# Kernel tuning notes

Hardware: AMD Instinct MI355X
Metric: run time of the kernel (lower is better)

The kernel has to match this reference:

```python
import jax, jax.numpy as jnp
import numpy as np

N_NODES = 50000
N_EDGES = 800000
IN_CH = 128
HID = 64
HEADS = 4
OUT_CH = 12
NEG_SLOPE = 0.2


def setup_inputs() -> dict:
    key = jax.random.key(0)
    ks = jax.random.split(key, 16)
    s = 0.05
    F1 = HEADS * HID  # 256
    return {
        "x": jax.random.normal(ks[0], (N_NODES, IN_CH), jnp.float32),
        "edge_index": jax.random.randint(ks[1], (2, N_EDGES), 0, N_NODES, jnp.int64 if jax.config.jax_enable_x64 else jnp.int32),
        # GAT layer 1 params
        "W1": jax.random.normal(ks[2], (IN_CH, F1), jnp.float32) * s,
        "att_src1": jax.random.normal(ks[3], (HEADS, HID), jnp.float32) * s,
        "att_dst1": jax.random.normal(ks[4], (HEADS, HID), jnp.float32) * s,
        "b1": jnp.zeros((F1,), jnp.float32),
        # GAT layer 2 params
        "W2": jax.random.normal(ks[5], (F1, F1), jnp.float32) * s,
        "att_src2": jax.random.normal(ks[6], (HEADS, HID), jnp.float32) * s,
        "att_dst2": jax.random.normal(ks[7], (HEADS, HID), jnp.float32) * s,
        "b2": jnp.zeros((F1,), jnp.float32),
        # temporal Conv1d(F1 -> HID, k=3, pad=1)
        "conv_w": jax.random.normal(ks[8], (HID, F1, 3), jnp.float32) * s,
        "conv_b": jnp.zeros((HID,), jnp.float32),
        # final Linear(HID -> OUT_CH)
        "lin_w": jax.random.normal(ks[9], (HID, OUT_CH), jnp.float32) * s,
        "lin_b": jnp.zeros((OUT_CH,), jnp.float32),
    }


def _gat_layer(x, src, dst, W, a_src, a_dst, bias):
    # x: [N, Fin]; src/dst: [E] (self-loops already included)
    h = (x @ W).reshape(x.shape[0], HEADS, HID)          # [N, H, C]
    alpha_s = jnp.sum(h * a_src[None], axis=-1)          # [N, H]
    alpha_d = jnp.sum(h * a_dst[None], axis=-1)          # [N, H]
    e = jax.nn.leaky_relu(alpha_s[src] + alpha_d[dst], NEG_SLOPE)  # [E, H]
    # segment softmax over destination nodes
    m = jax.ops.segment_max(e, dst, num_segments=N_NODES)          # [N, H]
    ex = jnp.exp(e - m[dst])
    denom = jax.ops.segment_sum(ex, dst, num_segments=N_NODES)
    alpha = ex / (denom[dst] + 1e-16)                    # [E, H]
    msg = h[src] * alpha[:, :, None]                     # [E, H, C]
    out = jax.ops.segment_sum(msg, dst, num_segments=N_NODES)      # [N, H, C]
    return out.reshape(N_NODES, HEADS * HID) + bias


def reference(x, edge_index, W1, att_src1, att_dst1, b1, W2, att_src2, att_dst2, b2, conv_w, conv_b, lin_w, lin_b):
    # add self loops (PyG GATConv default)
    loops = jnp.arange(N_NODES, dtype=edge_index.dtype)
    src = jnp.concatenate([edge_index[0], loops])
    dst = jnp.concatenate([edge_index[1], loops])

    h = jax.nn.relu(_gat_layer(x, src, dst, W1, att_src1, att_dst1, b1))
    h = jax.nn.relu(_gat_layer(h, src, dst, W2, att_src2, att_dst2, b2))

    # temporal Conv1d over the node axis: [1, F1, N] -> [1, HID, N]
    inp = h.T[None]                                      # [1, F1, N]
    y = jax.lax.conv_general_dilated(inp, conv_w, (1,), [(1, 1)],
                                     dimension_numbers=("NCH", "OIH", "NCH"))
    y = jax.nn.relu(y + conv_b[None, :, None])           # [1, HID, N]
    out = y[0].T @ lin_w + lin_b                         # [N, OUT_CH]
    return out
```

## Files before the change

kernel.cpp:

```cpp
#include <hip/hip_runtime.h>
#include <hip/hip_bf16.h>

#define N_NODES 50000
#define N_EDGES 800000
#define E_TOT   (N_EDGES + N_NODES)
#define IN_CH   128
#define HID     64
#define HEADS   4
#define F1      256
#define OUT_CH  12
#define NEG_SLOPE 0.2f
#define CAP     256

typedef __attribute__((ext_vector_type(8))) short  bf16x8;
typedef __attribute__((ext_vector_type(4))) float  f32x4;

__device__ __forceinline__ float leaky(float x) { return x > 0.f ? x : NEG_SLOPE * x; }

__device__ __forceinline__ unsigned short tob(float f) {
    unsigned u = __float_as_uint(f);
    u += 0x7fffu + ((u >> 16) & 1u);
    return (unsigned short)(u >> 16);
}
__device__ __forceinline__ float fromb(unsigned short s) {
    return __uint_as_float(((unsigned)s) << 16);
}

__global__ void k_zero(int* p, int n) {
    int i = blockIdx.x * blockDim.x + threadIdx.x;
    if (i < n) p[i] = 0;
}

__global__ void k_count(const int* __restrict__ ei, int* __restrict__ counts) {
    int i = blockIdx.x * blockDim.x + threadIdx.x;
    if (i >= E_TOT) return;
    int dst = (i < N_EDGES) ? ei[N_EDGES + i] : (i - N_EDGES);
    atomicAdd(&counts[dst], 1);
}

__global__ __launch_bounds__(1024) void k_scan(const int* __restrict__ counts,
                                               int* __restrict__ rowptr,
                                               int* __restrict__ cursor) {
    __shared__ int wsum[16];
    __shared__ int carrysh;
    const int lane = threadIdx.x & 63, w = threadIdx.x >> 6;
    if (threadIdx.x == 0) carrysh = 0;
    __syncthreads();
    for (int base = 0; base < N_NODES; base += 1024) {
        int i = base + threadIdx.x;
        int v = (i < N_NODES) ? counts[i] : 0;
        int s = v;
        #pragma unroll
        for (int off = 1; off < 64; off <<= 1) {
            int t = __shfl_up(s, off);
            if (lane >= off) s += t;
        }
        if (lane == 63) wsum[w] = s;
        __syncthreads();
        int woff = 0;
        for (int j = 0; j < w; ++j) woff += wsum[j];
        int incl = carrysh + woff + s;
        if (i < N_NODES) { rowptr[i] = incl - v; cursor[i] = incl - v; }
        __syncthreads();
        if (threadIdx.x == 1023) carrysh = incl;
        __syncthreads();
    }
    if (threadIdx.x == 0) rowptr[N_NODES] = carrysh;
}

__global__ void k_fill(const int* __restrict__ ei, int* __restrict__ cursor,
                       int* __restrict__ csr_src) {
    int i = blockIdx.x * blockDim.x + threadIdx.x;
    if (i >= E_TOT) return;
    int src, dst;
    if (i < N_EDGES) { src = ei[i]; dst = ei[N_EDGES + i]; }
    else             { src = dst = i - N_EDGES; }
    int pos = atomicAdd(&cursor[dst], 1);
    csr_src[pos] = src;
}

__global__ void k_cast4(const float* __restrict__ in, unsigned short* __restrict__ out, int n4) {
    int i = blockIdx.x * blockDim.x + threadIdx.x;
    if (i >= n4) return;
    float4 v = *(const float4*)&in[i * 4];
    ushort4 o;
    o.x = tob(v.x); o.y = tob(v.y); o.z = tob(v.z); o.w = tob(v.w);
    *(ushort4*)&out[i * 4] = o;
}

__global__ void k_prep_wt(const float* __restrict__ W, unsigned short* __restrict__ WT,
                          int K, int N) {
    int idx = blockIdx.x * blockDim.x + threadIdx.x;
    if (idx >= K * N) return;
    int n = idx / K, k = idx % K;
    WT[idx] = tob(W[(size_t)k * N + n]);
}

__global__ void k_prep_cw(const float* __restrict__ CW, unsigned short* __restrict__ BT) {
    int idx = blockIdx.x * blockDim.x + threadIdx.x;
    if (idx >= 64 * 768) return;
    int o = idx / 768, kk = idx % 768;
    int kseg = kk >> 8, c = kk & 255;
    BT[idx] = tob(CW[((size_t)o * 256 + c) * 3 + kseg]);
}

__global__ __launch_bounds__(256) void k_gemm_bf16(const unsigned short* __restrict__ A,
                                                   const unsigned short* __restrict__ BT,
                                                   unsigned short* __restrict__ C,
                                                   int M, int K) {
    __shared__ unsigned short As[128][40];
    __shared__ unsigned short Bs[128][40];
    const int t    = threadIdx.x;
    const int lane = t & 63, wave = t >> 6;
    const int wr = wave >> 1, wc = wave & 1;
    const int row0 = blockIdx.y * 128, col0 = blockIdx.x * 128;
    const int r = t & 127, half = t >> 7;
    const int l15 = lane & 15, kg = lane >> 4;

    f32x4 acc[4][4];
    #pragma unroll
    for (int m = 0; m < 4; ++m)
        #pragma unroll
        for (int n = 0; n < 4; ++n) acc[m][n] = 0.f;

    for (int k0 = 0; k0 < K; k0 += 32) {
        int ar = row0 + r;
        uint4 av0 = make_uint4(0, 0, 0, 0), av1 = make_uint4(0, 0, 0, 0);
        if (ar < M) {
            const unsigned short* ap = &A[(size_t)ar * K + k0 + half * 16];
            av0 = *(const uint4*)ap;
            av1 = *(const uint4*)(ap + 8);
        }
        *(uint4*)&As[r][half * 16]     = av0;
        *(uint4*)&As[r][half * 16 + 8] = av1;
        const unsigned short* bp = &BT[(size_t)(col0 + r) * K + k0 + half * 16];
        uint4 bv0 = *(const uint4*)bp;
        uint4 bv1 = *(const uint4*)(bp + 8);
        *(uint4*)&Bs[r][half * 16]     = bv0;
        *(uint4*)&Bs[r][half * 16 + 8] = bv1;
        __syncthreads();
        bf16x8 af[4], bf[4];
        #pragma unroll
        for (int m = 0; m < 4; ++m) af[m] = *(const bf16x8*)&As[wr * 64 + m * 16 + l15][kg * 8];
        #pragma unroll
        for (int n = 0; n < 4; ++n) bf[n] = *(const bf16x8*)&Bs[wc * 64 + n * 16 + l15][kg * 8];
        #pragma unroll
        for (int m = 0; m < 4; ++m)
            #pragma unroll
            for (int n = 0; n < 4; ++n)
                acc[m][n] = __builtin_amdgcn_mfma_f32_16x16x32_bf16(af[m], bf[n], acc[m][n], 0, 0, 0);
        __syncthreads();
    }
    #pragma unroll
    for (int m = 0; m < 4; ++m) {
        #pragma unroll
        for (int j = 0; j < 4; ++j) {
            int row = row0 + wr * 64 + m * 16 + (lane >> 4) * 4 + j;
            if (row < M) {
                #pragma unroll
                for (int n = 0; n < 4; ++n)
                    C[(size_t)row * F1 + col0 + wc * 64 + n * 16 + l15] = tob(acc[m][n][j]);
            }
        }
    }
}

__global__ __launch_bounds__(256) void k_attn(const unsigned short* __restrict__ H,
                                              const float* __restrict__ a_src,
                                              const float* __restrict__ a_dst,
                                              float* __restrict__ oS,
                                              float* __restrict__ oD) {
    int lane = threadIdx.x & 63, wid = threadIdx.x >> 6;
    int node = blockIdx.x * 4 + wid;
    int head = lane >> 4, cc = (lane & 15) * 4;
    ushort4 hv4 = *(const ushort4*)&H[(size_t)node * F1 + lane * 4];
    float h0 = fromb(hv4.x), h1 = fromb(hv4.y), h2 = fromb(hv4.z), h3 = fromb(hv4.w);
    float4 sv = *(const float4*)&a_src[head * HID + cc];
    float4 dv = *(const float4*)&a_dst[head * HID + cc];
    float s = h0 * sv.x + h1 * sv.y + h2 * sv.z + h3 * sv.w;
    float d = h0 * dv.x + h1 * dv.y + h2 * dv.z + h3 * dv.w;
    #pragma unroll
    for (int off = 1; off < 16; off <<= 1) {
        s += __shfl_xor(s, off);
        d += __shfl_xor(d, off);
    }
    if ((lane & 15) == 0) { oS[node * 4 + head] = s; oD[node * 4 + head] = d; }
}

__global__ __launch_bounds__(256) void k_agg(const unsigned short* __restrict__ H,
                                             const float* __restrict__ aS,
                                             const float* __restrict__ aD,
                                             const int* __restrict__ rowptr,
                                             const int* __restrict__ csr,
                                             const float* __restrict__ bias,
                                             unsigned short* __restrict__ O) {
    __shared__ float wlds[4][CAP][4];
    int lane = threadIdx.x & 63, wid = threadIdx.x >> 6;
    int node = blockIdx.x * 4 + wid;
    int beg = rowptr[node], end = rowptr[node + 1];

    float4 adv = *(const float4*)&aD[node * 4];
    float ad[4] = { adv.x, adv.y, adv.z, adv.w };
    float m[4] = { -1e30f, -1e30f, -1e30f, -1e30f };
    float s[4] = { 0.f, 0.f, 0.f, 0.f };

    for (int j = beg + lane; j < end; j += 64) {
        int src = csr[j];
        float4 asv = *(const float4*)&aS[src * 4];
        float as4[4] = { asv.x, asv.y, asv.z, asv.w };
        #pragma unroll
        for (int h = 0; h < 4; ++h) {
            float e  = leaky(as4[h] + ad[h]);
            float mn = fmaxf(m[h], e);
            s[h] = s[h] * __expf(m[h] - mn) + __expf(e - mn);
            m[h] = mn;
        }
    }
    #pragma unroll
    for (int off = 1; off < 64; off <<= 1) {
        #pragma unroll
        for (int h = 0; h < 4; ++h) {
            float mo = __shfl_xor(m[h], off);
            float so = __shfl_xor(s[h], off);
            float mn = fmaxf(m[h], mo);
            s[h] = s[h] * __expf(m[h] - mn) + so * __expf(mo - mn);
            m[h] = mn;
        }
    }
    float inv4[4];
    #pragma unroll
    for (int h = 0; h < 4; ++h) inv4[h] = 1.f / (s[h] + 1e-16f);

    for (int j = beg + lane, idx = lane; j < end && idx < CAP; j += 64, idx += 64) {
        int src = csr[j];
        float4 asv = *(const float4*)&aS[src * 4];
        float4 w4;
        w4.x = __expf(leaky(asv.x + ad[0]) - m[0]) * inv4[0];
        w4.y = __expf(leaky(asv.y + ad[1]) - m[1]) * inv4[1];
        w4.z = __expf(leaky(asv.z + ad[2]) - m[2]) * inv4[2];
        w4.w = __expf(leaky(asv.w + ad[3]) - m[3]) * inv4[3];
        *(float4*)&wlds[wid][idx][0] = w4;
    }

    int   hl   = lane >> 4;
    float mh   = m[hl];
    float invh = inv4[hl];
    float adh  = ad[hl];
    float a0 = 0.f, a1 = 0.f, a2 = 0.f, a3 = 0.f;
    int deg  = end - beg;
    int degc = deg < CAP ? deg : CAP;
    for (int idx = 0; idx < degc; ++idx) {
        int src = csr[beg + idx];
        float w = wlds[wid][idx][hl];
        ushort4 hv = *(const ushort4*)&H[(size_t)src * F1 + lane * 4];
        a0 += w * fromb(hv.x); a1 += w * fromb(hv.y);
        a2 += w * fromb(hv.z); a3 += w * fromb(hv.w);
    }
    for (int idx = CAP; idx < deg; ++idx) {
        int src = csr[beg + idx];
        float e = leaky(aS[src * 4 + hl] + adh);
        float w = __expf(e - mh) * invh;
        ushort4 hv = *(const ushort4*)&H[(size_t)src * F1 + lane * 4];
        a0 += w * fromb(hv.x); a1 += w * fromb(hv.y);
        a2 += w * fromb(hv.z); a3 += w * fromb(hv.w);
    }
    float4 bv = *(const float4*)&bias[lane * 4];
    ushort4 o;
    o.x = tob(fmaxf(a0 + bv.x, 0.f));
    o.y = tob(fmaxf(a1 + bv.y, 0.f));
    o.z = tob(fmaxf(a2 + bv.z, 0.f));
    o.w = tob(fmaxf(a3 + bv.w, 0.f));
    *(ushort4*)&O[(size_t)node * F1 + lane * 4] = o;
}

__global__ __launch_bounds__(256) void k_conv(const unsigned short* __restrict__ H,
                                              const unsigned short* __restrict__ BcT,
                                              const float* __restrict__ CB,
                                              float* __restrict__ Y) {
    __shared__ unsigned short As[128][40];
    __shared__ unsigned short Bs[64][40];
    const int t    = threadIdx.x;
    const int lane = t & 63, wave = t >> 6;
    const int row0 = blockIdx.x * 128;
    const int r = t & 127, half = t >> 7;
    const int l15 = lane & 15, kg = lane >> 4;

    f32x4 acc[2][4];
    #pragma unroll
    for (int m = 0; m < 2; ++m)
        #pragma unroll
        for (int n = 0; n < 4; ++n) acc[m][n] = 0.f;

    for (int k0 = 0; k0 < 768; k0 += 32) {
        int kseg = k0 >> 8;
        int cbase = (k0 & 255) + half * 16;
        int gr = row0 + r + kseg - 1;
        uint4 av0 = make_uint4(0, 0, 0, 0), av1 = make_uint4(0, 0, 0, 0);
        if (gr >= 0 && gr < N_NODES) {
            const unsigned short* hp = &H[(size_t)gr * F1 + cbase];
            av0 = *(const uint4*)hp;
            av1 = *(const uint4*)(hp + 8);
        }
        *(uint4*)&As[r][half * 16]     = av0;
        *(uint4*)&As[r][half * 16 + 8] = av1;
        if (t < 128) {
            int br = t & 63, bh = t >> 6;
            const unsigned short* bp = &BcT[(size_t)br * 768 + k0 + bh * 16];
            uint4 bv0 = *(const uint4*)bp;
            uint4 bv1 = *(const uint4*)(bp + 8);
            *(uint4*)&Bs[br][bh * 16]     = bv0;
            *(uint4*)&Bs[br][bh * 16 + 8] = bv1;
        }
        __syncthreads();
        bf16x8 af[2], bf[4];
        #pragma unroll
        for (int m = 0; m < 2; ++m) af[m] = *(const bf16x8*)&As[wave * 32 + m * 16 + l15][kg * 8];
        #pragma unroll
        for (int n = 0; n < 4; ++n) bf[n] = *(const bf16x8*)&Bs[n * 16 + l15][kg * 8];
        #pragma unroll
        for (int m = 0; m < 2; ++m)
            #pragma unroll
            for (int n = 0; n < 4; ++n)
                acc[m][n] = __builtin_amdgcn_mfma_f32_16x16x32_bf16(af[m], bf[n], acc[m][n], 0, 0, 0);
        __syncthreads();
    }
    #pragma unroll
    for (int m = 0; m < 2; ++m) {
        #pragma unroll
        for (int j = 0; j < 4; ++j) {
            int row = row0 + wave * 32 + m * 16 + (lane >> 4) * 4 + j;
            if (row < N_NODES) {
                #pragma unroll
                for (int n = 0; n < 4; ++n) {
                    int col = n * 16 + l15;
                    Y[(size_t)row * HID + col] = fmaxf(acc[m][n][j] + CB[col], 0.f);
                }
            }
        }
    }
}

__global__ __launch_bounds__(256) void k_lin(const float* __restrict__ Y,
                                             const float* __restrict__ LW,
                                             const float* __restrict__ LB,
                                             float* __restrict__ OUT) {
    __shared__ float w[64][12];
    __shared__ float b[12];
    for (int i = threadIdx.x; i < 64 * 12; i += 256) w[i / 12][i % 12] = LW[i];
    if (threadIdx.x < 12) b[threadIdx.x] = LB[threadIdx.x];
    __syncthreads();
    int n = blockIdx.x * 256 + threadIdx.x;
    if (n >= N_NODES) return;
    float acc[12];
    #pragma unroll
    for (int o = 0; o < 12; ++o) acc[o] = b[o];
    for (int c = 0; c < 64; c += 4) {
        float4 yv = *(const float4*)&Y[(size_t)n * HID + c];
        #pragma unroll
        for (int o = 0; o < 12; ++o)
            acc[o] += yv.x * w[c][o] + yv.y * w[c + 1][o]
                    + yv.z * w[c + 2][o] + yv.w * w[c + 3][o];
    }
    #pragma unroll
    for (int o = 0; o < 12; ++o) OUT[(size_t)n * OUT_CH + o] = acc[o];
}

extern "C" void kernel_launch(void* const* d_in, const int* in_sizes, int n_in,
                              void* d_out, int out_size, void* d_ws, size_t ws_size,
                              hipStream_t stream) {
    const float* x   = (const float*)d_in[0];
    const int*   ei  = (const int*)d_in[1];
    const float* W1  = (const float*)d_in[2];
    const float* as1 = (const float*)d_in[3];
    const float* ad1 = (const float*)d_in[4];
    const float* b1  = (const float*)d_in[5];
    const float* W2  = (const float*)d_in[6];
    const float* as2 = (const float*)d_in[7];
    const float* ad2 = (const float*)d_in[8];
    const float* b2  = (const float*)d_in[9];
    const float* cw  = (const float*)d_in[10];
    const float* cb  = (const float*)d_in[11];
    const float* lw  = (const float*)d_in[12];
    const float* lb  = (const float*)d_in[13];
    float* out = (float*)d_out;

    char* ws = (char*)d_ws;
    size_t off = 0;
    auto alloc = [&](size_t bytes) -> void* {
        off = (off + 255) & ~(size_t)255;
        void* p = ws + off;
        off += bytes;
        return p;
    };
    unsigned short* hA  = (unsigned short*)alloc((size_t)N_NODES * F1 * 2);
    unsigned short* hB  = (unsigned short*)alloc((size_t)N_NODES * F1 * 2);
    unsigned short* xb  = (unsigned short*)alloc((size_t)N_NODES * IN_CH * 2);
    unsigned short* wt1 = (unsigned short*)alloc((size_t)F1 * IN_CH * 2);
    unsigned short* wt2 = (unsigned short*)alloc((size_t)F1 * F1 * 2);
    unsigned short* cwt = (unsigned short*)alloc((size_t)HID * 768 * 2);
    float* alS    = (float*)alloc((size_t)N_NODES * 4 * 4);
    float* alD    = (float*)alloc((size_t)N_NODES * 4 * 4);
    int*   counts = (int*)  alloc((size_t)N_NODES * 4);
    int*   rowptr = (int*)  alloc((size_t)(N_NODES + 1) * 4);
    int*   cursor = (int*)  alloc((size_t)N_NODES * 4);
    int*   csr    = (int*)  alloc((size_t)E_TOT * 4);
    float* y      = (float*)alloc((size_t)N_NODES * HID * 4);

    k_zero <<<(N_NODES + 255) / 256, 256, 0, stream>>>(counts, N_NODES);
    k_count<<<(E_TOT + 255) / 256, 256, 0, stream>>>(ei, counts);
    k_scan <<<1, 1024, 0, stream>>>(counts, rowptr, cursor);
    k_fill <<<(E_TOT + 255) / 256, 256, 0, stream>>>(ei, cursor, csr);

    k_cast4 <<<(N_NODES * IN_CH / 4 + 255) / 256, 256, 0, stream>>>(x, xb, N_NODES * IN_CH / 4);
    k_prep_wt<<<(IN_CH * F1 + 255) / 256, 256, 0, stream>>>(W1, wt1, IN_CH, F1);
    k_prep_wt<<<(F1 * F1 + 255) / 256, 256, 0, stream>>>(W2, wt2, F1, F1);
    k_prep_cw<<<(HID * 768 + 255) / 256, 256, 0, stream>>>(cw, cwt);

    dim3 gg(F1 / 128, (N_NODES + 127) / 128);
    k_gemm_bf16<<<gg, 256, 0, stream>>>(xb, wt1, hA, N_NODES, IN_CH);
    k_attn<<<N_NODES / 4, 256, 0, stream>>>(hA, as1, ad1, alS, alD);
    k_agg <<<N_NODES / 4, 256, 0, stream>>>(hA, alS, alD, rowptr, csr, b1, hB);
    k_gemm_bf16<<<gg, 256, 0, stream>>>(hB, wt2, hA, N_NODES, F1);
    k_attn<<<N_NODES / 4, 256, 0, stream>>>(hA, as2, ad2, alS, alD);
    k_agg <<<N_NODES / 4, 256, 0, stream>>>(hA, alS, alD, rowptr, csr, b2, hB);
    k_conv<<<(N_NODES + 127) / 128, 256, 0, stream>>>(hB, cwt, cb, y);
    k_lin <<<(N_NODES + 255) / 256, 256, 0, stream>>>(y, lw, lb, out);
}
```

Measured before the change: 483.9 us.

## Use direct global-to-LDS loads in GEMM/conv and restructure softmax in aggregation

The GEMM and conv kernels now stage their tiles with global_load_lds 16-byte direct loads instead of loading through registers and storing to shared memory. The LDS padding is dropped to fit that layout. The conv input gets zeroed guard rows so boundary checks can go. The aggregation kernel caches edge logits in LDS and finds the max in one pass, computes the exps and sum in a second pass, and applies the normalisation once at the end. This trades the per-edge online-softmax rescaling for extra LDS traffic. Removing the padding may add LDS bank conflicts on the MFMA fragment reads.

```diff
diff --git a/kernel.cpp b/kernel.cpp
--- a/kernel.cpp
+++ b/kernel.cpp
@@ -26,9 +26,21 @@
     return __uint_as_float(((unsigned)s) << 16);
 }
 
+typedef __attribute__((address_space(3))) unsigned int        lds_u32;
+typedef const __attribute__((address_space(1))) unsigned int  glb_u32;
+__device__ __forceinline__ void gload16(const void* g, void* l) {
+    __builtin_amdgcn_global_load_lds((glb_u32*)g, (lds_u32*)l, 16, 0, 0);
+}
+
 __global__ void k_zero(int* p, int n) {
     int i = blockIdx.x * blockDim.x + threadIdx.x;
     if (i < n) p[i] = 0;
+}
+
+__global__ void k_guard(unsigned int* front, unsigned int* back) {
+    int i = threadIdx.x;
+    if (i < 128) front[i] = 0;
+    else         back[i - 128] = 0;
 }
 
 __global__ void k_count(const int* __restrict__ ei, int* __restrict__ counts) {
@@ -108,15 +120,23 @@
                                                    const unsigned short* __restrict__ BT,
                                                    unsigned short* __restrict__ C,
                                                    int M, int K) {
-    __shared__ unsigned short As[128][40];
-    __shared__ unsigned short Bs[128][40];
+    __shared__ unsigned short As[128][32];
+    __shared__ unsigned short Bs[128][32];
     const int t    = threadIdx.x;
     const int lane = t & 63, wave = t >> 6;
     const int wr = wave >> 1, wc = wave & 1;
     const int row0 = blockIdx.y * 128, col0 = blockIdx.x * 128;
-    const int r = t & 127, half = t >> 7;
     const int l15 = lane & 15, kg = lane >> 4;
 
+    const int srow = (wave << 4) + (lane >> 2);
+    const int sseg = (lane & 3) * 8;
+    int ar0 = row0 + srow;      if (ar0 >= M) ar0 = M - 1;
+    int ar1 = row0 + srow + 64; if (ar1 >= M) ar1 = M - 1;
+    const int br0 = col0 + srow, br1 = col0 + srow + 64;
+    unsigned short* ldsA = &As[0][0];
+    unsigned short* ldsB = &Bs[0][0];
+    const int lofs0 = wave * 512, lofs1 = 2048 + wave * 512;
+
     f32x4 acc[4][4];
     #pragma unroll
     for (int m = 0; m < 4; ++m)
@@ -124,20 +144,10 @@
         for (int n = 0; n < 4; ++n) acc[m][n] = 0.f;
 
     for (int k0 = 0; k0 < K; k0 += 32) {
-        int ar = row0 + r;
-        uint4 av0 = make_uint4(0, 0, 0, 0), av1 = make_uint4(0, 0, 0, 0);
-        if (ar < M) {
-            const unsigned short* ap = &A[(size_t)ar * K + k0 + half * 16];
-            av0 = *(const uint4*)ap;
-            av1 = *(const uint4*)(ap + 8);
-        }
-        *(uint4*)&As[r][half * 16]     = av0;
-        *(uint4*)&As[r][half * 16 + 8] = av1;
-        const unsigned short* bp = &BT[(size_t)(col0 + r) * K + k0 + half * 16];
-        uint4 bv0 = *(const uint4*)bp;
-        uint4 bv1 = *(const uint4*)(bp + 8);
-        *(uint4*)&Bs[r][half * 16]     = bv0;
-        *(uint4*)&Bs[r][half * 16 + 8] = bv1;
+        gload16(&A [(size_t)ar0 * K + k0 + sseg], ldsA + lofs0);
+        gload16(&A [(size_t)ar1 * K + k0 + sseg], ldsA + lofs1);
+        gload16(&BT[(size_t)br0 * K + k0 + sseg], ldsB + lofs0);
+        gload16(&BT[(size_t)br1 * K + k0 + sseg], ldsB + lofs1);
         __syncthreads();
         bf16x8 af[4], bf[4];
         #pragma unroll
@@ -198,57 +208,59 @@
     int lane = threadIdx.x & 63, wid = threadIdx.x >> 6;
     int node = blockIdx.x * 4 + wid;
     int beg = rowptr[node], end = rowptr[node + 1];
+    int deg = end - beg;
 
     float4 adv = *(const float4*)&aD[node * 4];
     float ad[4] = { adv.x, adv.y, adv.z, adv.w };
     float m[4] = { -1e30f, -1e30f, -1e30f, -1e30f };
-    float s[4] = { 0.f, 0.f, 0.f, 0.f };
-
-    for (int j = beg + lane; j < end; j += 64) {
+
+    for (int j = beg + lane, idx = lane; j < end; j += 64, idx += 64) {
         int src = csr[j];
         float4 asv = *(const float4*)&aS[src * 4];
-        float as4[4] = { asv.x, asv.y, asv.z, asv.w };
-        #pragma unroll
-        for (int h = 0; h < 4; ++h) {
-            float e  = leaky(as4[h] + ad[h]);
-            float mn = fmaxf(m[h], e);
-            s[h] = s[h] * __expf(m[h] - mn) + __expf(e - mn);
-            m[h] = mn;
-        }
+        float4 e4;
+        e4.x = leaky(asv.x + ad[0]);
+        e4.y = leaky(asv.y + ad[1]);
+        e4.z = leaky(asv.z + ad[2]);
+        e4.w = leaky(asv.w + ad[3]);
+        m[0] = fmaxf(m[0], e4.x); m[1] = fmaxf(m[1], e4.y);
+        m[2] = fmaxf(m[2], e4.z); m[3] = fmaxf(m[3], e4.w);
+        if (idx < CAP) *(float4*)&wlds[wid][idx][0] = e4;
     }
     #pragma unroll
     for (int off = 1; off < 64; off <<= 1) {
         #pragma unroll
-        for (int h = 0; h < 4; ++h) {
-            float mo = __shfl_xor(m[h], off);
-            float so = __shfl_xor(s[h], off);
-            float mn = fmaxf(m[h], mo);
-            s[h] = s[h] * __expf(m[h] - mn) + so * __expf(mo - mn);
-            m[h] = mn;
-        }
-    }
-    float inv4[4];
-    #pragma unroll
-    for (int h = 0; h < 4; ++h) inv4[h] = 1.f / (s[h] + 1e-16f);
-
-    for (int j = beg + lane, idx = lane; j < end && idx < CAP; j += 64, idx += 64) {
+        for (int h = 0; h < 4; ++h) m[h] = fmaxf(m[h], __shfl_xor(m[h], off));
+    }
+
+    float s[4] = { 0.f, 0.f, 0.f, 0.f };
+    int degc = deg < CAP ? deg : CAP;
+    for (int idx = lane; idx < degc; idx += 64) {
+        float4 e4 = *(float4*)&wlds[wid][idx][0];
+        float4 w4;
+        w4.x = __expf(e4.x - m[0]); w4.y = __expf(e4.y - m[1]);
+        w4.z = __expf(e4.z - m[2]); w4.w = __expf(e4.w - m[3]);
+        s[0] += w4.x; s[1] += w4.y; s[2] += w4.z; s[3] += w4.w;
+        *(float4*)&wlds[wid][idx][0] = w4;
+    }
+    for (int j = beg + CAP + lane; j < end; j += 64) {
         int src = csr[j];
         float4 asv = *(const float4*)&aS[src * 4];
-        float4 w4;
-        w4.x = __expf(leaky(asv.x + ad[0]) - m[0]) * inv4[0];
-        w4.y = __expf(leaky(asv.y + ad[1]) - m[1]) * inv4[1];
-        w4.z = __expf(leaky(asv.z + ad[2]) - m[2]) * inv4[2];
-        w4.w = __expf(leaky(asv.w + ad[3]) - m[3]) * inv4[3];
-        *(float4*)&wlds[wid][idx][0] = w4;
+        s[0] += __expf(leaky(asv.x + ad[0]) - m[0]);
+        s[1] += __expf(leaky(asv.y + ad[1]) - m[1]);
+        s[2] += __expf(leaky(asv.z + ad[2]) - m[2]);
+        s[3] += __expf(leaky(asv.w + ad[3]) - m[3]);
+    }
+    #pragma unroll
+    for (int off = 1; off < 64; off <<= 1) {
+        #pragma unroll
+        for (int h = 0; h < 4; ++h) s[h] += __shfl_xor(s[h], off);
     }
 
     int   hl   = lane >> 4;
+    float invh = 1.f / (s[hl] + 1e-16f);
     float mh   = m[hl];
-    float invh = inv4[hl];
     float adh  = ad[hl];
     float a0 = 0.f, a1 = 0.f, a2 = 0.f, a3 = 0.f;
-    int deg  = end - beg;
-    int degc = deg < CAP ? deg : CAP;
     for (int idx = 0; idx < degc; ++idx) {
         int src = csr[beg + idx];
         float w = wlds[wid][idx][hl];
@@ -258,18 +270,17 @@
     }
     for (int idx = CAP; idx < deg; ++idx) {
         int src = csr[beg + idx];
-        float e = leaky(aS[src * 4 + hl] + adh);
-        float w = __expf(e - mh) * invh;
+        float w = __expf(leaky(aS[src * 4 + hl] + adh) - mh);
         ushort4 hv = *(const ushort4*)&H[(size_t)src * F1 + lane * 4];
         a0 += w * fromb(hv.x); a1 += w * fromb(hv.y);
         a2 += w * fromb(hv.z); a3 += w * fromb(hv.w);
     }
     float4 bv = *(const float4*)&bias[lane * 4];
     ushort4 o;
-    o.x = tob(fmaxf(a0 + bv.x, 0.f));
-    o.y = tob(fmaxf(a1 + bv.y, 0.f));
-    o.z = tob(fmaxf(a2 + bv.z, 0.f));
-    o.w = tob(fmaxf(a3 + bv.w, 0.f));
+    o.x = tob(fmaxf(a0 * invh + bv.x, 0.f));
+    o.y = tob(fmaxf(a1 * invh + bv.y, 0.f));
+    o.z = tob(fmaxf(a2 * invh + bv.z, 0.f));
+    o.w = tob(fmaxf(a3 * invh + bv.w, 0.f));
     *(ushort4*)&O[(size_t)node * F1 + lane * 4] = o;
 }
 
@@ -277,14 +288,19 @@
                                               const unsigned short* __restrict__ BcT,
                                               const float* __restrict__ CB,
                                               float* __restrict__ Y) {
-    __shared__ unsigned short As[128][40];
-    __shared__ unsigned short Bs[64][40];
+    __shared__ unsigned short As[128][32];
+    __shared__ unsigned short Bs[64][32];
     const int t    = threadIdx.x;
     const int lane = t & 63, wave = t >> 6;
     const int row0 = blockIdx.x * 128;
-    const int r = t & 127, half = t >> 7;
     const int l15 = lane & 15, kg = lane >> 4;
 
+    const int srow = (wave << 4) + (lane >> 2);
+    const int sseg = (lane & 3) * 8;
+    unsigned short* ldsA = &As[0][0];
+    unsigned short* ldsB = &Bs[0][0];
+    const int lofs0 = wave * 512, lofs1 = 2048 + wave * 512;
+
     f32x4 acc[2][4];
     #pragma unroll
     for (int m = 0; m < 2; ++m)
@@ -292,24 +308,16 @@
         for (int n = 0; n < 4; ++n) acc[m][n] = 0.f;
 
     for (int k0 = 0; k0 < 768; k0 += 32) {
-        int kseg = k0 >> 8;
-        int cbase = (k0 & 255) + half * 16;
-        int gr = row0 + r + kseg - 1;
-        uint4 av0 = make_uint4(0, 0, 0, 0), av1 = make_uint4(0, 0, 0, 0);
-        if (gr >= 0 && gr < N_NODES) {
-            const unsigned short* hp = &H[(size_t)gr * F1 + cbase];
-            av0 = *(const uint4*)hp;
-            av1 = *(const uint4*)(hp + 8);
-        }
-        *(uint4*)&As[r][half * 16]     = av0;
-        *(uint4*)&As[r][half * 16 + 8] = av1;
-        if (t < 128) {
-            int br = t & 63, bh = t >> 6;
-            const unsigned short* bp = &BcT[(size_t)br * 768 + k0 + bh * 16];
-            uint4 bv0 = *(const uint4*)bp;
-            uint4 bv1 = *(const uint4*)(bp + 8);
-            *(uint4*)&Bs[br][bh * 16]     = bv0;
-            *(uint4*)&Bs[br][bh * 16 + 8] = bv1;
+        int kseg  = k0 >> 8;
+        int cbase = (k0 & 255) + sseg;
+        int gr0 = row0 + srow + kseg - 1;
+        int gr1 = gr0 + 64;
+        if (gr1 > N_NODES) gr1 = N_NODES;
+        gload16(H + (ptrdiff_t)gr0 * F1 + cbase, ldsA + lofs0);
+        gload16(H + (ptrdiff_t)gr1 * F1 + cbase, ldsA + lofs1);
+        {
+            int brow = srow;
+            gload16(&BcT[(size_t)brow * 768 + k0 + sseg], ldsB + lofs0);
         }
         __syncthreads();
         bf16x8 af[2], bf[4];
@@ -393,7 +401,8 @@
         return p;
     };
     unsigned short* hA  = (unsigned short*)alloc((size_t)N_NODES * F1 * 2);
-    unsigned short* hB  = (unsigned short*)alloc((size_t)N_NODES * F1 * 2);
+    unsigned short* hBg = (unsigned short*)alloc((size_t)(N_NODES + 2) * F1 * 2);
+    unsigned short* hB  = hBg + F1;
     unsigned short* xb  = (unsigned short*)alloc((size_t)N_NODES * IN_CH * 2);
     unsigned short* wt1 = (unsigned short*)alloc((size_t)F1 * IN_CH * 2);
     unsigned short* wt2 = (unsigned short*)alloc((size_t)F1 * F1 * 2);
@@ -407,6 +416,8 @@
     float* y      = (float*)alloc((size_t)N_NODES * HID * 4);
 
     k_zero <<<(N_NODES + 255) / 256, 256, 0, stream>>>(counts, N_NODES);
+    k_guard<<<1, 256, 0, stream>>>((unsigned int*)hBg,
+                                   (unsigned int*)(hBg + (size_t)(N_NODES + 1) * F1));
     k_count<<<(E_TOT + 255) / 256, 256, 0, stream>>>(ei, counts);
     k_scan <<<1, 1024, 0, stream>>>(counts, rowptr, cursor);
     k_fill <<<(E_TOT + 255) / 256, 256, 0, stream>>>(ei, cursor, csr);
```

New measurement: 468.9 us. 1.03x faster.
